# Kernel optimization log

Hardware: AMD Instinct MI355X
Metric: run time of the kernel (lower is better)

## Reference

```python
import jax, jax.numpy as jnp
import numpy as np

RADIUS = 0.1
KSIZE = 3          # kernel points per dimension
P_DIM = 3
K = KSIZE ** P_DIM  # 27 kernel points
KP_EXTENT = RADIUS / (KSIZE - 1) * P_DIM ** 0.5


def _kernel_points():
    # grid kernel points, same as getKernelPoints(radius, 3, dim=3)
    xyz = np.linspace(-1.0, 1.0, KSIZE)
    pts = np.meshgrid(*P_DIM * [xyz])
    pts = np.vstack([p.flatten() for p in pts]).T
    pts = pts / P_DIM ** 0.5
    return jnp.asarray(pts * RADIUS, dtype=jnp.float32)  # [K, 3]


def setup_inputs() -> dict:
    key = jax.random.key(0)
    k1, k2, k3, k4, k5 = jax.random.split(key, 5)
    N, S, H, CIN, COUT = 40000, 40000, 32, 64, 64
    # points in a [0, 0.2]^3 cube so neighbor offsets are comparable to radius
    q_pts = jax.random.uniform(k1, (N, 3), jnp.float32) * 0.2
    s_pts = jax.random.uniform(k2, (S, 3), jnp.float32) * 0.2
    neighb_inds = jax.random.randint(k3, (N, H), 0, S)
    x = jax.random.normal(k4, (S, CIN), jnp.float32)
    # kaiming-style init for the [K, Cin, Cout] grouped weights
    weights = jax.random.normal(k5, (K, CIN, COUT), jnp.float32) * (1.0 / np.sqrt(CIN))
    return {"q_pts": q_pts, "s_pts": s_pts, "neighb_inds": neighb_inds,
            "x": x, "weights": weights}


def reference(q_pts, s_pts, neighb_inds, x, weights):
    kp = _kernel_points()  # [K, 3], non-trainable constant
    # shadow padding row (sentinel point far away, zero feature)
    s_pad = jnp.concatenate([s_pts, jnp.full((1, s_pts.shape[-1]), 1e6, s_pts.dtype)], axis=0)
    x_pad = jnp.concatenate([x, jnp.zeros((1, x.shape[-1]), x.dtype)], axis=0)
    neighbors = s_pad[neighb_inds] - q_pts[:, None, :]      # [N, H, 3]
    neighb_x = x_pad[neighb_inds]                           # [N, H, Cin]
    # kernel-point influence weights: linear correlation clipped at 0
    diff = neighbors[:, :, None, :] - kp[None, None, :, :]  # [N, H, K, 3]
    sq_dist = jnp.sum(diff * diff, axis=-1)                 # [N, H, K]
    all_w = jnp.maximum(1.0 - jnp.sqrt(sq_dist) / KP_EXTENT, 0.0)
    # weighted grouped matmul over K kernel weight matrices
    fx = jnp.einsum('nhl,nhi,lio->no', all_w, neighb_x, weights)  # [N, Cout]
    return fx
```

## Files before the change

### kernel.cpp

```cpp
#include <hip/hip_runtime.h>

typedef _Float16 half_t;
typedef _Float16 half4_t __attribute__((ext_vector_type(4)));
typedef _Float16 half8   __attribute__((ext_vector_type(8)));
typedef float    f32x4   __attribute__((ext_vector_type(4)));
typedef unsigned short u16x8 __attribute__((ext_vector_type(8)));

#define KP_S    0.057735026918962574f
#define INV_EXT 11.547005383792515f
#define GPITCH  3616
#define BQ      16

__global__ void build_wt(const float* __restrict__ W, half_t* __restrict__ WT) {
    int t = blockIdx.x * 256 + threadIdx.x;
    if (t >= 64 * 1792) return;
    int o = t / 1792, k = t - o * 1792;
    int i = k / 28,   l = k - i * 28;
    WT[t] = (l < 27) ? (half_t)W[(l * 64 + i) * 64 + o] : (half_t)0.f;
}

__global__ __launch_bounds__(512, 4) void kpconv(
    const float* __restrict__ q_pts, const float* __restrict__ s_pts,
    const int*   __restrict__ inds,  const float* __restrict__ x,
    const half_t* __restrict__ WT,   float* __restrict__ out)
{
    __shared__ __align__(16) char   g_mem[BQ * GPITCH];
    __shared__ __align__(16) unsigned short idx_lds[BQ][32];
    __shared__ __align__(16) f32x4  red[4][64];

    const int tid  = threadIdx.x;
    const int lane = tid & 63, wid = tid >> 6;
    const int lr   = lane & 15, g = lane >> 4;
    const int base = blockIdx.x * BQ;

    {
        int q = tid >> 5, h = tid & 31;
        int n = base + q;
        int idx = inds[n * 32 + h];
        idx_lds[q][h] = (unsigned short)idx;
        f32x4 v;
        v.x = s_pts[idx * 3 + 0] - q_pts[n * 3 + 0];
        v.y = s_pts[idx * 3 + 1] - q_pts[n * 3 + 1];
        v.z = s_pts[idx * 3 + 2] - q_pts[n * 3 + 2];
        v.w = 0.f;
        *(f32x4*)(g_mem + q * GPITCH + h * 16) = v;
    }
    __syncthreads();

    const float kx0 = (float)((lr / 3) % 3 - 1) * KP_S;
    const float ky0 = (float)( lr / 9      - 1) * KP_S;
    const float kz0 = (float)( lr % 3      - 1) * KP_S;
    const int   l1  = lr + 16;
    const bool  hv1 = (l1 < 27);
    const float kx1 = (float)((l1 / 3) % 3 - 1) * KP_S;
    const float ky1 = (float)( l1 / 9      - 1) * KP_S;
    const float kz1 = (float)( l1 % 3      - 1) * KP_S;

    for (int qq = 0; qq < 2; ++qq) {
        const int q = wid * 2 + qq;
        char* gq = g_mem + q * GPITCH;

        u16x8 id8 = *(const u16x8*)&idx_lds[q][8 * g];
        float xv[32];
        #pragma unroll
        for (int j = 0; j < 8; ++j) {
            const float* xp = x + (int)id8[j] * 64 + lr;
            #pragma unroll
            for (int nt = 0; nt < 4; ++nt) xv[nt * 8 + j] = xp[16 * nt];
        }

        half8 a0, a1;
        #pragma unroll
        for (int j = 0; j < 8; ++j) {
            f32x4 nb = *(const f32x4*)(gq + (8 * g + j) * 16);
            float dx = nb.x - kx0, dy = nb.y - ky0, dz = nb.z - kz0;
            float s0 = dx * dx + dy * dy + dz * dz;
            a0[j] = (half_t)fmaxf(1.f - sqrtf(s0) * INV_EXT, 0.f);
            float ex = nb.x - kx1, ey = nb.y - ky1, ez = nb.z - kz1;
            float s1 = ex * ex + ey * ey + ez * ez;
            float w1 = fmaxf(1.f - sqrtf(s1) * INV_EXT, 0.f);
            a1[j] = (half_t)(hv1 ? w1 : 0.f);
        }

        #pragma unroll
        for (int nt = 0; nt < 4; ++nt) {
            half8 b;
            #pragma unroll
            for (int j = 0; j < 8; ++j) b[j] = (half_t)xv[nt * 8 + j];
            f32x4 z = {0.f, 0.f, 0.f, 0.f};
            f32x4 c0 = __builtin_amdgcn_mfma_f32_16x16x32_f16(a0, b, z, 0, 0, 0);
            f32x4 c1 = __builtin_amdgcn_mfma_f32_16x16x32_f16(a1, b, z, 0, 0, 0);
            int i = 16 * nt + lr;
            half4_t h0;
            h0[0] = (half_t)c0[0]; h0[1] = (half_t)c0[1];
            h0[2] = (half_t)c0[2]; h0[3] = (half_t)c0[3];
            *(half4_t*)(gq + 2 * (i * 28 + 4 * g)) = h0;
            int lb1 = 16 + 4 * g;
            if (lb1 < 28) {
                half4_t h1;
                h1[0] = (half_t)c1[0]; h1[1] = (half_t)c1[1];
                h1[2] = (half_t)c1[2]; h1[3] = (half_t)c1[3];
                *(half4_t*)(gq + 2 * (i * 28 + lb1)) = h1;
            }
        }
    }
    __syncthreads();

    {
        const int ot = wid & 3, kh = wid >> 2;
        const half_t* wrow = WT + (16 * ot + lr) * 1792 + kh * 896 + 8 * g;
        const char*   gb   = g_mem + lr * GPITCH + kh * 1792;
        f32x4 accA = {0.f, 0.f, 0.f, 0.f}, accB = {0.f, 0.f, 0.f, 0.f};
        #pragma unroll 7
        for (int s = 0; s < 28; s += 2) {
            half8 aA = *(const half8*)(gb + 64 * s + 16 * g);
            half8 bA = *(const half8*)(wrow + 32 * s);
            accA = __builtin_amdgcn_mfma_f32_16x16x32_f16(aA, bA, accA, 0, 0, 0);
            half8 aB = *(const half8*)(gb + 64 * (s + 1) + 16 * g);
            half8 bB = *(const half8*)(wrow + 32 * (s + 1));
            accB = __builtin_amdgcn_mfma_f32_16x16x32_f16(aB, bB, accB, 0, 0, 0);
        }
        f32x4 acc = accA + accB;
        if (kh == 1) *(f32x4*)&red[ot][lane] = acc;
        __syncthreads();
        if (kh == 0) {
            f32x4 p = red[ot][lane];
            acc.x += p.x; acc.y += p.y; acc.z += p.z; acc.w += p.w;
            int o = 16 * ot + lr;
            #pragma unroll
            for (int r = 0; r < 4; ++r)
                out[(base + 4 * g + r) * 64 + o] = acc[r];
        }
    }
}

extern "C" void kernel_launch(void* const* d_in, const int* in_sizes, int n_in,
                              void* d_out, int out_size, void* d_ws, size_t ws_size,
                              hipStream_t stream) {
    const float* q_pts = (const float*)d_in[0];
    const float* s_pts = (const float*)d_in[1];
    const int*   inds  = (const int*)d_in[2];
    const float* x     = (const float*)d_in[3];
    const float* W     = (const float*)d_in[4];
    float* out = (float*)d_out;
    half_t* WT = (half_t*)d_ws;

    build_wt<<<448, 256, 0, stream>>>(W, WT);
    kpconv<<<2500, 512, 0, stream>>>(q_pts, s_pts, inds, x, WT, out);
}
```

Measured before the change: 108.6 us.

## Make kpconv persistent with double-buffered prefetch of next tile's gathers

Changes the kernel from one block per 16-query tile to 512 persistent blocks looping over tiles. Neighbor indices, offsets and gathered feature values for the next tile are prefetched into double-buffered LDS and register arrays while the current tile's MFMA work runs, to hide global gather latency. It also uses packed fp16 conversions, hardware sqrt and a bias trick that replaces the kernel-point validity select. The risk is register pressure from two 64-float prefetch arrays under launch bounds of 512x4, plus load imbalance because 2500 tiles do not divide evenly over 512 blocks.

Result: slower. 255.3 us (+135.2%).

```diff
diff --git a/kernel.cpp b/kernel.cpp
--- a/kernel.cpp
+++ b/kernel.cpp
@@ -1,6 +1,7 @@
 #include <hip/hip_runtime.h>
 
 typedef _Float16 half_t;
+typedef __fp16   fp16x2 __attribute__((ext_vector_type(2)));
 typedef _Float16 half4_t __attribute__((ext_vector_type(4)));
 typedef _Float16 half8   __attribute__((ext_vector_type(8)));
 typedef float    f32x4   __attribute__((ext_vector_type(4)));
@@ -9,7 +10,11 @@
 #define KP_S    0.057735026918962574f
 #define INV_EXT 11.547005383792515f
 #define GPITCH  3616
-#define BQ      16
+#define NBLK    512
+#define NTILE   2500
+
+union H8 { half8 v; fp16x2 h2[4]; };
+union H4 { half4_t v; fp16x2 h2[2]; };
 
 __global__ void build_wt(const float* __restrict__ W, half_t* __restrict__ WT) {
     int t = blockIdx.x * 256 + threadIdx.x;
@@ -19,118 +24,151 @@
     WT[t] = (l < 27) ? (half_t)W[(l * 64 + i) * 64 + o] : (half_t)0.f;
 }
 
+#define ISSUE_XV(BUF, XV) do {                                                 \
+    u16x8 idA = *(const u16x8*)&idx_lds[BUF][2 * wid][8 * g];                  \
+    u16x8 idB = *(const u16x8*)&idx_lds[BUF][2 * wid + 1][8 * g];              \
+    _Pragma("unroll")                                                          \
+    for (int j = 0; j < 8; ++j) {                                              \
+        const float* pa = x + (int)idA[j] * 64 + lr;                           \
+        const float* pb = x + (int)idB[j] * 64 + lr;                           \
+        _Pragma("unroll")                                                      \
+        for (int nt = 0; nt < 4; ++nt) {                                       \
+            XV[nt * 8 + j]      = pa[16 * nt];                                 \
+            XV[32 + nt * 8 + j] = pb[16 * nt];                                 \
+        }                                                                      \
+    }                                                                          \
+} while (0)
+
+#define BODY(T, TN, CUR, XVIN, XVOUT) do {                                     \
+                                            \
+    const int nn   = (TN) * 16 + aq;                                           \
+    const int idxN = inds[nn * 32 + ah];                                       \
+                \
+    _Pragma("unroll")                                                          \
+    for (int qq = 0; qq < 2; ++qq) {                                           \
+        const int q = wid * 2 + qq;                                            \
+        float w0v[8], w1v[8];                                                  \
+        _Pragma("unroll")                                                      \
+        for (int j = 0; j < 8; ++j) {                                          \
+            f32x4 nb = nbr_lds[CUR][q][8 * g + j];                             \
+            float dx = nb.x - kx0, dy = nb.y - ky0, dz = nb.z - kz0;           \
+            w0v[j] = fmaxf(fmaf(__builtin_amdgcn_sqrtf(dx*dx + dy*dy + dz*dz), -INV_EXT, 1.f), 0.f); \
+            float ex = nb.x - kx1, ey = nb.y - ky1, ez = nb.z - kz1;           \
+            w1v[j] = fmaxf(fmaf(__builtin_amdgcn_sqrtf(ex*ex + ey*ey + ez*ez), -INV_EXT, cbias), 0.f); \
+        }                                                                      \
+        H8 A0, A1;                                                             \
+        _Pragma("unroll")                                                      \
+        for (int p = 0; p < 4; ++p) {                                          \
+            A0.h2[p] = __builtin_amdgcn_cvt_pkrtz(w0v[2*p], w0v[2*p+1]);       \
+            A1.h2[p] = __builtin_amdgcn_cvt_pkrtz(w1v[2*p], w1v[2*p+1]);       \
+        }                                                                      \
+        char* gq = g_mem + q * GPITCH;                                         \
+        _Pragma("unroll")                                                      \
+        for (int nt = 0; nt < 4; ++nt) {                                       \
+            H8 B;                                                              \
+            _Pragma("unroll")                                                  \
+            for (int p = 0; p < 4; ++p)                                        \
+                B.h2[p] = __builtin_amdgcn_cvt_pkrtz(XVIN[qq*32 + nt*8 + 2*p], \
+                                                     XVIN[qq*32 + nt*8 + 2*p + 1]); \
+            f32x4 z = {0.f, 0.f, 0.f, 0.f};                                    \
+            f32x4 c0 = __builtin_amdgcn_mfma_f32_16x16x32_f16(A0.v, B.v, z, 0, 0, 0); \
+            f32x4 c1 = __builtin_amdgcn_mfma_f32_16x16x32_f16(A1.v, B.v, z, 0, 0, 0); \
+            const int ic = 16 * nt + lr;                                       \
+            H4 h0;                                                             \
+            h0.h2[0] = __builtin_amdgcn_cvt_pkrtz(c0[0], c0[1]);               \
+            h0.h2[1] = __builtin_amdgcn_cvt_pkrtz(c0[2], c0[3]);               \
+            *(half4_t*)(gq + 2 * (ic * 28 + 4 * g)) = h0.v;                    \
+            if (4 * g < 12) {                                                  \
+                H4 h1;                                                         \
+                h1.h2[0] = __builtin_amdgcn_cvt_pkrtz(c1[0], c1[1]);           \
+                h1.h2[1] = __builtin_amdgcn_cvt_pkrtz(c1[2], c1[3]);           \
+                *(half4_t*)(gq + 2 * (ic * 28 + 16 + 4 * g)) = h1.v;           \
+            }                                                                  \
+        }                                                                      \
+    }                                                                          \
+                                        \
+    f32x4 vN;                                                                  \
+    vN.x = s_pts[idxN * 3 + 0] - q_pts[nn * 3 + 0];                            \
+    vN.y = s_pts[idxN * 3 + 1] - q_pts[nn * 3 + 1];                            \
+    vN.z = s_pts[idxN * 3 + 2] - q_pts[nn * 3 + 2];                            \
+    vN.w = 0.f;                                                                \
+    idx_lds[(CUR) ^ 1][aq][ah] = (unsigned short)idxN;                         \
+    __syncthreads();                                                  \
+    ISSUE_XV((CUR) ^ 1, XVOUT);                                       \
+         \
+    const half_t* wrow = WT + (16 * ot + lr) * 1792 + kh * 896 + 8 * g;        \
+    const char*   gb   = g_mem + lr * GPITCH + kh * 1792;                      \
+    f32x4 accA = {0.f, 0.f, 0.f, 0.f}, accB = {0.f, 0.f, 0.f, 0.f};            \
+    _Pragma("unroll 7")                                                        \
+    for (int s = 0; s < 28; s += 2) {                                          \
+        half8 aA = *(const half8*)(gb + 64 * s + 16 * g);                      \
+        half8 bA = *(const half8*)(wrow + 32 * s);                             \
+        accA = __builtin_amdgcn_mfma_f32_16x16x32_f16(aA, bA, accA, 0, 0, 0);  \
+        half8 aB = *(const half8*)(gb + 64 * (s + 1) + 16 * g);                \
+        half8 bB = *(const half8*)(wrow + 32 * (s + 1));                       \
+        accB = __builtin_amdgcn_mfma_f32_16x16x32_f16(aB, bB, accB, 0, 0, 0);  \
+    }                                                                          \
+    f32x4 acc = accA + accB;                                                   \
+    if (kh) *(f32x4*)&red[ot][lane] = acc;                                     \
+    nbr_lds[(CUR) ^ 1][aq][ah] = vN;                                  \
+    __syncthreads();                                                  \
+    if (!kh) {                                                        \
+        f32x4 p = red[ot][lane];                                               \
+        const int o = 16 * ot + lr;                                            \
+        _Pragma("unroll")                                                      \
+        for (int r = 0; r < 4; ++r)                                            \
+            out[((T) * 16 + 4 * g + r) * 64 + o] = acc[r] + p[r];              \
+    }                                                                          \
+} while (0)
+
 __global__ __launch_bounds__(512, 4) void kpconv(
     const float* __restrict__ q_pts, const float* __restrict__ s_pts,
     const int*   __restrict__ inds,  const float* __restrict__ x,
     const half_t* __restrict__ WT,   float* __restrict__ out)
 {
-    __shared__ __align__(16) char   g_mem[BQ * GPITCH];
-    __shared__ __align__(16) unsigned short idx_lds[BQ][32];
+    __shared__ __align__(16) char   g_mem[16 * GPITCH];
+    __shared__ __align__(16) unsigned short idx_lds[2][16][32];
+    __shared__ __align__(16) f32x4  nbr_lds[2][16][32];
     __shared__ __align__(16) f32x4  red[4][64];
 
     const int tid  = threadIdx.x;
     const int lane = tid & 63, wid = tid >> 6;
     const int lr   = lane & 15, g = lane >> 4;
-    const int base = blockIdx.x * BQ;
+    const int aq   = tid >> 5,  ah = tid & 31;
+    const int ot   = wid & 3,   kh = wid >> 2;
+
+    const float kx0 = (float)((lr / 3) % 3 - 1) * KP_S;
+    const float ky0 = (float)( lr / 9      - 1) * KP_S;
+    const float kz0 = (float)( lr % 3      - 1) * KP_S;
+    const int   l1  = lr + 16;
+    const float kx1 = (float)((l1 / 3) % 3 - 1) * KP_S;
+    const float ky1 = (float)( l1 / 9      - 1) * KP_S;
+    const float kz1 = (float)( l1 % 3      - 1) * KP_S;
+    const float cbias = (l1 < 27) ? 1.f : -1.f;
 
     {
-        int q = tid >> 5, h = tid & 31;
-        int n = base + q;
-        int idx = inds[n * 32 + h];
-        idx_lds[q][h] = (unsigned short)idx;
+        int n   = blockIdx.x * 16 + aq;
+        int idx = inds[n * 32 + ah];
+        idx_lds[0][aq][ah] = (unsigned short)idx;
         f32x4 v;
         v.x = s_pts[idx * 3 + 0] - q_pts[n * 3 + 0];
         v.y = s_pts[idx * 3 + 1] - q_pts[n * 3 + 1];
         v.z = s_pts[idx * 3 + 2] - q_pts[n * 3 + 2];
         v.w = 0.f;
-        *(f32x4*)(g_mem + q * GPITCH + h * 16) = v;
+        nbr_lds[0][aq][ah] = v;
     }
     __syncthreads();
 
-    const float kx0 = (float)((lr / 3) % 3 - 1) * KP_S;
-    const float ky0 = (float)( lr / 9      - 1) * KP_S;
-    const float kz0 = (float)( lr % 3      - 1) * KP_S;
-    const int   l1  = lr + 16;
-    const bool  hv1 = (l1 < 27);
-    const float kx1 = (float)((l1 / 3) % 3 - 1) * KP_S;
-    const float ky1 = (float)( l1 / 9      - 1) * KP_S;
-    const float kz1 = (float)( l1 % 3      - 1) * KP_S;
+    float xvA[64], xvB[64];
+    ISSUE_XV(0, xvA);
 
-    for (int qq = 0; qq < 2; ++qq) {
-        const int q = wid * 2 + qq;
-        char* gq = g_mem + q * GPITCH;
-
-        u16x8 id8 = *(const u16x8*)&idx_lds[q][8 * g];
-        float xv[32];
-        #pragma unroll
-        for (int j = 0; j < 8; ++j) {
-            const float* xp = x + (int)id8[j] * 64 + lr;
-            #pragma unroll
-            for (int nt = 0; nt < 4; ++nt) xv[nt * 8 + j] = xp[16 * nt];
-        }
-
-        half8 a0, a1;
-        #pragma unroll
-        for (int j = 0; j < 8; ++j) {
-            f32x4 nb = *(const f32x4*)(gq + (8 * g + j) * 16);
-            float dx = nb.x - kx0, dy = nb.y - ky0, dz = nb.z - kz0;
-            float s0 = dx * dx + dy * dy + dz * dz;
-            a0[j] = (half_t)fmaxf(1.f - sqrtf(s0) * INV_EXT, 0.f);
-            float ex = nb.x - kx1, ey = nb.y - ky1, ez = nb.z - kz1;
-            float s1 = ex * ex + ey * ey + ez * ez;
-            float w1 = fmaxf(1.f - sqrtf(s1) * INV_EXT, 0.f);
-            a1[j] = (half_t)(hv1 ? w1 : 0.f);
-        }
-
-        #pragma unroll
-        for (int nt = 0; nt < 4; ++nt) {
-            half8 b;
-            #pragma unroll
-            for (int j = 0; j < 8; ++j) b[j] = (half_t)xv[nt * 8 + j];
-            f32x4 z = {0.f, 0.f, 0.f, 0.f};
-            f32x4 c0 = __builtin_amdgcn_mfma_f32_16x16x32_f16(a0, b, z, 0, 0, 0);
-            f32x4 c1 = __builtin_amdgcn_mfma_f32_16x16x32_f16(a1, b, z, 0, 0, 0);
-            int i = 16 * nt + lr;
-            half4_t h0;
-            h0[0] = (half_t)c0[0]; h0[1] = (half_t)c0[1];
-            h0[2] = (half_t)c0[2]; h0[3] = (half_t)c0[3];
-            *(half4_t*)(gq + 2 * (i * 28 + 4 * g)) = h0;
-            int lb1 = 16 + 4 * g;
-            if (lb1 < 28) {
-                half4_t h1;
-                h1[0] = (half_t)c1[0]; h1[1] = (half_t)c1[1];
-                h1[2] = (half_t)c1[2]; h1[3] = (half_t)c1[3];
-                *(half4_t*)(gq + 2 * (i * 28 + lb1)) = h1;
-            }
-        }
-    }
-    __syncthreads();
-
-    {
-        const int ot = wid & 3, kh = wid >> 2;
-        const half_t* wrow = WT + (16 * ot + lr) * 1792 + kh * 896 + 8 * g;
-        const char*   gb   = g_mem + lr * GPITCH + kh * 1792;
-        f32x4 accA = {0.f, 0.f, 0.f, 0.f}, accB = {0.f, 0.f, 0.f, 0.f};
-        #pragma unroll 7
-        for (int s = 0; s < 28; s += 2) {
-            half8 aA = *(const half8*)(gb + 64 * s + 16 * g);
-            half8 bA = *(const half8*)(wrow + 32 * s);
-            accA = __builtin_amdgcn_mfma_f32_16x16x32_f16(aA, bA, accA, 0, 0, 0);
-            half8 aB = *(const half8*)(gb + 64 * (s + 1) + 16 * g);
-            half8 bB = *(const half8*)(wrow + 32 * (s + 1));
-            accB = __builtin_amdgcn_mfma_f32_16x16x32_f16(aB, bB, accB, 0, 0, 0);
-        }
-        f32x4 acc = accA + accB;
-        if (kh == 1) *(f32x4*)&red[ot][lane] = acc;
-        __syncthreads();
-        if (kh == 0) {
-            f32x4 p = red[ot][lane];
-            acc.x += p.x; acc.y += p.y; acc.z += p.z; acc.w += p.w;
-            int o = 16 * ot + lr;
-            #pragma unroll
-            for (int r = 0; r < 4; ++r)
-                out[(base + 4 * g + r) * 64 + o] = acc[r];
-        }
+    int cur = 0, useA = 1;
+    for (int t = blockIdx.x; t < NTILE; t += NBLK) {
+        int tn = (t + NBLK < NTILE) ? t + NBLK : t;
+        if (useA) { BODY(t, tn, cur, xvA, xvB); }
+        else      { BODY(t, tn, cur, xvB, xvA); }
+        useA ^= 1;
+        cur  ^= 1;
     }
 }
 
@@ -146,5 +184,5 @@
     half_t* WT = (half_t*)d_ws;
 
     build_wt<<<448, 256, 0, stream>>>(W, WT);
-    kpconv<<<2500, 512, 0, stream>>>(q_pts, s_pts, inds, x, WT, out);
+    kpconv<<<NBLK, 512, 0, stream>>>(q_pts, s_pts, inds, x, WT, out);
 }
```
